# Kernel optimization log

Measured on AMD Instinct MI355X. Metric: run time of the kernel, lower is better.

## Reference

```python
import jax, jax.numpy as jnp
import numpy as np

B, N, C_IN, C_OUT = 32, 4096, 16, 64
EMB, LINK, WIN = 16, 3, 12


def setup_inputs() -> dict:
    key = jax.random.key(0)
    ks = jax.random.split(key, 7)
    s = lambda k, shape, sc=1.0: jax.random.normal(k, shape, dtype=jnp.float32) * sc
    return {
        "x": s(ks[0], (B, N, C_IN)),
        "x_window": s(ks[1], (B, WIN, N, C_IN)),
        "node_embeddings": s(ks[2], (N, EMB)),
        "weights_pool": s(ks[3], (EMB, LINK, C_IN, C_OUT), 0.1),
        "weights_window": s(ks[4], (EMB, C_IN, C_OUT), 0.1),
        "bias_pool": s(ks[5], (EMB, C_OUT), 0.1),
        "T": s(ks[6], (WIN,), 0.1),
    }


def reference(x, x_window, node_embeddings, weights_pool, weights_window, bias_pool, T):
    # Adaptive adjacency: softmax over rows of relu(E E^T)   [N, N]
    n = node_embeddings.shape[0]
    supports = jax.nn.softmax(
        jax.nn.relu(node_embeddings @ node_embeddings.T), axis=1)
    # Chebyshev polynomial hops: T0=I, T1=A, Tk = 2*A*T(k-1) - T(k-2)
    support_set = [jnp.eye(n, dtype=supports.dtype), supports]
    for _ in range(2, weights_pool.shape[1]):
        support_set.append(2.0 * (supports @ support_set[-1]) - support_set[-2])
    supports_k = jnp.stack(support_set, axis=0)  # [K, N, N]

    # Per-node weight generation from node embeddings
    weights = jnp.einsum('nd,dkio->nkio', node_embeddings, weights_pool)  # [N,K,Cin,Cout]
    bias = node_embeddings @ bias_pool  # [N, Cout]

    # Multi-hop spatial graph convolution
    x_g = jnp.einsum('knm,bmc->bnkc', supports_k, x)  # [B, N, K, Cin]
    x_gconv = jnp.einsum('bnki,nkio->bno', x_g, weights) + bias  # [B, N, Cout]

    # Temporal window transformation: time-mix with T, per-node weights
    x_w = jnp.einsum('btni,t->bni', x_window, T)  # [B, N, Cin]
    w_win = jnp.einsum('nd,dio->nio', node_embeddings, weights_window)  # [N,Cin,Cout]
    x_wconv = jnp.einsum('bni,nio->bno', x_w, w_win)  # [B, N, Cout]

    return x_gconv + x_wconv
```

## Files before the change

kernel.cpp:

```cpp
#include <hip/hip_runtime.h>
#include <hip/hip_bf16.h>

#define NN 4096
#define BB 32
#define CIN 16
#define COUT 64
#define EMB 16
#define KLINK 3
#define WWIN 12
#define BCIN (BB * CIN)
#define KSPLIT 4

typedef unsigned short ushort_t;
typedef __attribute__((ext_vector_type(8))) short bf16x8;
typedef __attribute__((ext_vector_type(4))) float f32x4;
typedef __attribute__((ext_vector_type(4))) unsigned short us4;
typedef __attribute__((ext_vector_type(8))) unsigned short us8;

static __device__ __forceinline__ ushort_t f2bf(float f) {
  union { float f; unsigned u; } v; v.f = f;
  const unsigned r = v.u + 0x7fffu + ((v.u >> 16) & 1u);
  return (ushort_t)(r >> 16);
}
static __device__ __forceinline__ float bf2f(ushort_t u) {
  union { unsigned u; float f; } v; v.u = ((unsigned)u) << 16;
  return v.f;
}

__device__ __forceinline__ void gload16(const void* g, void* l) {
  __builtin_amdgcn_global_load_lds(
      (const __attribute__((address_space(1))) void*)g,
      (__attribute__((address_space(3))) void*)l, 16, 0, 0);
}

__global__ __launch_bounds__(256) void prep_kernel(
    const float* __restrict__ E, const float* __restrict__ Wp,
    const float* __restrict__ Wwp, const float* __restrict__ biasp,
    ushort_t* __restrict__ Ebf, ushort_t* __restrict__ Wpct,
    float* __restrict__ biasn, float* __restrict__ r) {
  const int gid = blockIdx.x * 256 + threadIdx.x;
  if (gid < NN) {
    r[gid] = 0.0f;
    const float* e = E + (size_t)gid * EMB;
    ushort_t* o = Ebf + (size_t)gid * 32;
    #pragma unroll
    for (int d = 0; d < 16; ++d) o[d] = f2bf(e[d]);
    #pragma unroll
    for (int d = 16; d < 32; ++d) o[d] = 0;
  } else if (gid < 2 * NN) {
    const int j = gid - NN;
    const int oo = j >> 6;
    const int i = j & 63;
    const int q = i >> 4;
    const int ii = i & 15;
    ushort_t* w = Wpct + (size_t)j * 32;
    #pragma unroll
    for (int d = 0; d < 16; ++d) {
      float v;
      if (q == 0)
        v = Wp[((size_t)(d * 3 + 0) * 16 + ii) * 64 + oo] -
            Wp[((size_t)(d * 3 + 2) * 16 + ii) * 64 + oo];
      else if (q == 1)
        v = Wp[((size_t)(d * 3 + 1) * 16 + ii) * 64 + oo];
      else if (q == 2)
        v = 2.0f * Wp[((size_t)(d * 3 + 2) * 16 + ii) * 64 + oo];
      else
        v = Wwp[((size_t)d * 16 + ii) * 64 + oo];
      w[d] = f2bf(v);
    }
    #pragma unroll
    for (int d = 16; d < 32; ++d) w[d] = 0;
  } else {
    const int t = gid - 2 * NN;
    if (t < NN * 16) {
      const int n = t >> 4;
      const int o4 = t & 15;
      const float4* bp4 = reinterpret_cast<const float4*>(biasp);
      float4 acc = make_float4(0.f, 0.f, 0.f, 0.f);
      #pragma unroll
      for (int d = 0; d < 16; ++d) {
        const float e = E[(size_t)n * EMB + d];
        const float4 b = bp4[d * 16 + o4];
        acc.x += e * b.x; acc.y += e * b.y; acc.z += e * b.z; acc.w += e * b.w;
      }
      *reinterpret_cast<float4*>(biasn + (size_t)n * 64 + o4 * 4) = acc;
    }
  }
}

__global__ __launch_bounds__(256) void gemm_mfma_kernel(
    const ushort_t* __restrict__ Ag, const ushort_t* __restrict__ Bt,
    ushort_t* __restrict__ Ct, int lda, int ldb, int ldc, int Kdim,
    const float* __restrict__ rowR, const float* __restrict__ colR) {
  __shared__ ushort_t As[128 * 32];
  __shared__ ushort_t Bs[64 * 32];
  const int tid = threadIdx.x;
  const int lane = tid & 63;
  const int wid = tid >> 6;
  const int wr = wid >> 1;
  const int wc = wid & 1;
  const int row0 = blockIdx.y * 128;
  const int col0 = blockIdx.x * 64;

  f32x4 acc[4][2];
  #pragma unroll
  for (int i = 0; i < 4; ++i)
    #pragma unroll
    for (int j = 0; j < 2; ++j) acc[i][j] = (f32x4){0.f, 0.f, 0.f, 0.f};

  const int sr = tid >> 2;
  const int scs = (((tid & 3) ^ (sr & 3)) * 8);
  const ushort_t* agp0 = Ag + (size_t)(row0 + sr) * lda + scs;
  const ushort_t* agp1 = Ag + (size_t)(row0 + 64 + sr) * lda + scs;
  const ushort_t* bgp  = Bt + (size_t)(col0 + sr) * ldb + scs;
  ushort_t* asl0 = &As[tid * 8];
  ushort_t* asl1 = &As[2048 + tid * 8];
  ushort_t* bsl  = &Bs[tid * 8];

  const int kq = (lane >> 4) * 8;
  const int fr = lane & 15;

  for (int kb = 0; kb < Kdim; kb += 32) {
    gload16(agp0 + kb, asl0);
    gload16(agp1 + kb, asl1);
    gload16(bgp + kb, bsl);
    __syncthreads();

    bf16x8 af[4], bfr[2];
    #pragma unroll
    for (int i = 0; i < 4; ++i) {
      const int r = wr * 64 + i * 16 + fr;
      af[i] = *reinterpret_cast<const bf16x8*>(&As[r * 32 + (kq ^ ((r & 3) * 8))]);
    }
    #pragma unroll
    for (int j = 0; j < 2; ++j) {
      const int r = wc * 32 + j * 16 + fr;
      bfr[j] = *reinterpret_cast<const bf16x8*>(&Bs[r * 32 + (kq ^ ((r & 3) * 8))]);
    }
    #pragma unroll
    for (int i = 0; i < 4; ++i)
      #pragma unroll
      for (int j = 0; j < 2; ++j)
        acc[i][j] = __builtin_amdgcn_mfma_f32_16x16x32_bf16(af[i], bfr[j],
                                                            acc[i][j], 0, 0, 0);
    __syncthreads();
  }

  #pragma unroll
  for (int i = 0; i < 4; ++i) {
    const int rg = row0 + wr * 64 + i * 16 + ((lane >> 4) << 2);
    float4 ri = make_float4(1.f, 1.f, 1.f, 1.f);
    if (rowR) {
      const float4 rv = *reinterpret_cast<const float4*>(&rowR[rg]);
      ri.x = 1.0f / rv.x; ri.y = 1.0f / rv.y;
      ri.z = 1.0f / rv.z; ri.w = 1.0f / rv.w;
    }
    #pragma unroll
    for (int j = 0; j < 2; ++j) {
      const int cg = col0 + wc * 32 + j * 16 + (lane & 15);
      float cs = 1.0f;
      if (colR) cs = 1.0f / colR[cg];
      us4 o;
      o.x = f2bf(acc[i][j][0] * ri.x * cs);
      o.y = f2bf(acc[i][j][1] * ri.y * cs);
      o.z = f2bf(acc[i][j][2] * ri.z * cs);
      o.w = f2bf(acc[i][j][3] * ri.w * cs);
      *reinterpret_cast<us4*>(&Ct[(size_t)cg * ldc + rg]) = o;
    }
  }
}

__global__ __launch_bounds__(256) void gemm_splitk_kernel(
    const ushort_t* __restrict__ Ag, const ushort_t* __restrict__ Bt,
    float* __restrict__ Cp, int lda, int ldb, int ldc, int kchunk) {
  __shared__ ushort_t As[2][128 * 32];
  __shared__ ushort_t Bs[2][64 * 32];
  const int tid = threadIdx.x;
  const int lane = tid & 63;
  const int wid = tid >> 6;
  const int wr = wid >> 1;
  const int wc = wid & 1;

  const int gx = gridDim.x, gy = gridDim.y;
  const int nwg = gx * gy * gridDim.z;
  int L = blockIdx.x + gx * (blockIdx.y + gy * blockIdx.z);
  L = (L & 7) * (nwg >> 3) + (L >> 3);
  const int bx = L % gx;
  const int by = (L / gx) % gy;
  const int bz = L / (gx * gy);

  const int row0 = by * 128;
  const int col0 = bx * 64;
  const int kbase = bz * kchunk;

  f32x4 acc[4][2];
  #pragma unroll
  for (int i = 0; i < 4; ++i)
    #pragma unroll
    for (int j = 0; j < 2; ++j) acc[i][j] = (f32x4){0.f, 0.f, 0.f, 0.f};

  const int sr = tid >> 2;
  const int scs = (((tid & 3) ^ (sr & 3)) * 8);
  const ushort_t* agp0 = Ag + (size_t)(row0 + sr) * lda + scs;
  const ushort_t* agp1 = Ag + (size_t)(row0 + 64 + sr) * lda + scs;
  const ushort_t* bgp  = Bt + (size_t)(col0 + sr) * ldb + scs;

  const int kq = (lane >> 4) * 8;
  const int fr = lane & 15;
  const int nt = kchunk >> 5;

  gload16(agp0 + kbase, &As[0][tid * 8]);
  gload16(agp1 + kbase, &As[0][2048 + tid * 8]);
  gload16(bgp + kbase, &Bs[0][tid * 8]);
  __syncthreads();

  int cur = 0;
  #pragma unroll 2
  for (int t = 0; t < nt; ++t) {
    const int nxt = cur ^ 1;
    if (t + 1 < nt) {
      const int kb = kbase + (t + 1) * 32;
      gload16(agp0 + kb, &As[nxt][tid * 8]);
      gload16(agp1 + kb, &As[nxt][2048 + tid * 8]);
      gload16(bgp + kb, &Bs[nxt][tid * 8]);
    }
    bf16x8 af[4], bfr[2];
    #pragma unroll
    for (int i = 0; i < 4; ++i) {
      const int r = wr * 64 + i * 16 + fr;
      af[i] = *reinterpret_cast<const bf16x8*>(
          &As[cur][r * 32 + (kq ^ ((r & 3) * 8))]);
    }
    #pragma unroll
    for (int j = 0; j < 2; ++j) {
      const int r = wc * 32 + j * 16 + fr;
      bfr[j] = *reinterpret_cast<const bf16x8*>(
          &Bs[cur][r * 32 + (kq ^ ((r & 3) * 8))]);
    }
    #pragma unroll
    for (int i = 0; i < 4; ++i)
      #pragma unroll
      for (int j = 0; j < 2; ++j)
        acc[i][j] = __builtin_amdgcn_mfma_f32_16x16x32_bf16(af[i], bfr[j],
                                                            acc[i][j], 0, 0, 0);
    __syncthreads();
    cur = nxt;
  }

  float* cpz = Cp + (size_t)bz * ((size_t)BCIN * NN);
  #pragma unroll
  for (int i = 0; i < 4; ++i) {
    const int rg = row0 + wr * 64 + i * 16 + ((lane >> 4) << 2);
    #pragma unroll
    for (int j = 0; j < 2; ++j) {
      const int cg = col0 + wc * 32 + j * 16 + (lane & 15);
      *reinterpret_cast<f32x4*>(&cpz[(size_t)cg * ldc + rg]) = acc[i][j];
    }
  }
}

__global__ __launch_bounds__(256) void reduce_splitk_kernel(
    const float* __restrict__ Cp, ushort_t* __restrict__ Ct,
    const float* __restrict__ R, int mode) {
  const size_t e = ((size_t)blockIdx.x * 256 + threadIdx.x) << 2;
  const size_t SS = (size_t)BCIN * NN;
  float4 s = *reinterpret_cast<const float4*>(Cp + e);
  #pragma unroll
  for (int z = 1; z < KSPLIT; ++z) {
    const float4 v = *reinterpret_cast<const float4*>(Cp + (size_t)z * SS + e);
    s.x += v.x; s.y += v.y; s.z += v.z; s.w += v.w;
  }
  if (mode == 0) {
    const float4 rv = *reinterpret_cast<const float4*>(R + (e & (NN - 1)));
    s.x /= rv.x; s.y /= rv.y; s.z /= rv.z; s.w /= rv.w;
  } else {
    const float ri = 1.0f / R[e >> 9];
    s.x *= ri; s.y *= ri; s.z *= ri; s.w *= ri;
  }
  us4 o;
  o.x = f2bf(s.x); o.y = f2bf(s.y); o.z = f2bf(s.z); o.w = f2bf(s.w);
  *reinterpret_cast<us4*>(Ct + e) = o;
}

__global__ __launch_bounds__(256) void pgemm_kernel(
    const ushort_t* __restrict__ Ebf, ushort_t* __restrict__ Pb,
    float* __restrict__ r) {
  __shared__ ushort_t As[128 * 32];
  __shared__ ushort_t Bs[64 * 32];
  const int tid = threadIdx.x;
  const int lane = tid & 63;
  const int wid = tid >> 6;
  const int wr = wid >> 1;
  const int wc = wid & 1;
  const int row0 = blockIdx.y * 128;
  const int col0 = blockIdx.x * 64;

  const int sr = tid >> 2;
  const int scs = (((tid & 3) ^ (sr & 3)) * 8);
  gload16(Ebf + (size_t)(row0 + sr) * 32 + scs, &As[tid * 8]);
  gload16(Ebf + (size_t)(row0 + 64 + sr) * 32 + scs, &As[2048 + tid * 8]);
  gload16(Ebf + (size_t)(col0 + sr) * 32 + scs, &Bs[tid * 8]);
  __syncthreads();

  const int kq = (lane >> 4) * 8;
  const int fr = lane & 15;
  bf16x8 af[4], bfr[2];
  #pragma unroll
  for (int i = 0; i < 4; ++i) {
    const int rr = wr * 64 + i * 16 + fr;
    af[i] = *reinterpret_cast<const bf16x8*>(&As[rr * 32 + (kq ^ ((rr & 3) * 8))]);
  }
  #pragma unroll
  for (int j = 0; j < 2; ++j) {
    const int rr = wc * 32 + j * 16 + fr;
    bfr[j] = *reinterpret_cast<const bf16x8*>(&Bs[rr * 32 + (kq ^ ((rr & 3) * 8))]);
  }
  f32x4 acc[4][2];
  #pragma unroll
  for (int i = 0; i < 4; ++i)
    #pragma unroll
    for (int j = 0; j < 2; ++j) acc[i][j] = (f32x4){0.f, 0.f, 0.f, 0.f};
  #pragma unroll
  for (int i = 0; i < 4; ++i)
    #pragma unroll
    for (int j = 0; j < 2; ++j)
      acc[i][j] = __builtin_amdgcn_mfma_f32_16x16x32_bf16(af[i], bfr[j],
                                                          acc[i][j], 0, 0, 0);

  float pv[4][2][4];
  #pragma unroll
  for (int i = 0; i < 4; ++i) {
    const int rg = row0 + wr * 64 + i * 16 + ((lane >> 4) << 2);
    #pragma unroll
    for (int j = 0; j < 2; ++j) {
      const int cg = col0 + wc * 32 + j * 16 + (lane & 15);
      us4 o;
      #pragma unroll
      for (int q = 0; q < 4; ++q) {
        const float p = __expf(fmaxf(acc[i][j][q], 0.0f) - 16.0f);
        pv[i][j][q] = p;
        o[q] = f2bf(p);
      }
      *reinterpret_cast<us4*>(&Pb[(size_t)cg * NN + rg]) = o;
    }
  }
  #pragma unroll
  for (int i = 0; i < 4; ++i) {
    const int rg = row0 + wr * 64 + i * 16 + ((lane >> 4) << 2);
    #pragma unroll
    for (int q = 0; q < 4; ++q) {
      float s = pv[i][0][q] + pv[i][1][q];
      s += __shfl_xor(s, 1, 64);
      s += __shfl_xor(s, 2, 64);
      s += __shfl_xor(s, 4, 64);
      s += __shfl_xor(s, 8, 64);
      if ((lane & 15) == 0) atomicAdd(&r[rg + q], s);
    }
  }
}

__global__ __launch_bounds__(256) void transpose_x_kernel(
    const float* __restrict__ x, ushort_t* __restrict__ XtT) {
  __shared__ ushort_t T[16][72];
  const int b = blockIdx.y;
  const int m0 = blockIdx.x * 64;
  const int tid = threadIdx.x;
  const int i = tid & 15;
  const int ml = tid >> 4;
  #pragma unroll
  for (int it = 0; it < 4; ++it) {
    const int m = m0 + ml + it * 16;
    T[i][ml + it * 16] = f2bf(x[((size_t)b * NN + m) * CIN + i]);
  }
  __syncthreads();
  if (tid < 128) {
    const int r = tid >> 3;
    const int c8 = (tid & 7) * 8;
    const us8 v = *reinterpret_cast<const us8*>(&T[r][c8]);
    *reinterpret_cast<us8*>(&XtT[(size_t)(b * CIN + r) * NN + m0 + c8]) = v;
  }
}

__global__ __launch_bounds__(256) void transpose_y1_kernel(
    const ushort_t* __restrict__ Y1T, ushort_t* __restrict__ Y1n) {
  __shared__ ushort_t T[64][72];
  const int c0 = blockIdx.x * 64;
  const int r0 = blockIdx.y * 64;
  const int tid = threadIdx.x;
  #pragma unroll
  for (int t = 0; t < 2; ++t) {
    const int lin = tid + t * 256;
    const int row = lin >> 3;
    const int ch = lin & 7;
    const us8 v = *reinterpret_cast<const us8*>(
        Y1T + (size_t)(r0 + row) * NN + c0 + ch * 8);
    *reinterpret_cast<us8*>(&T[row][ch * 8]) = v;
  }
  __syncthreads();
  #pragma unroll
  for (int t = 0; t < 2; ++t) {
    const int lin = tid + t * 256;
    const int cc = lin >> 3;
    const int ch = lin & 7;
    us8 v;
    #pragma unroll
    for (int e = 0; e < 8; ++e) v[e] = T[ch * 8 + e][cc];
    *reinterpret_cast<us8*>(Y1n + (size_t)(c0 + cc) * BCIN + r0 + ch * 8) = v;
  }
}

__global__ __launch_bounds__(256) void time_mix_kernel(
    const float* __restrict__ xw, const float* __restrict__ Tv,
    float* __restrict__ XW) {
  const int idx = blockIdx.x * 256 + threadIdx.x;
  if (idx >= BB * NN * 4) return;
  const int c4 = (idx & 3) << 2;
  const int nn = (idx >> 2) & (NN - 1);
  const int b = idx >> 14;
  float4 acc = make_float4(0.f, 0.f, 0.f, 0.f);
  #pragma unroll
  for (int t = 0; t < WWIN; ++t) {
    const float4 v = *reinterpret_cast<const float4*>(
        xw + (((size_t)b * WWIN + t) * NN + nn) * CIN + c4);
    const float tv = Tv[t];
    acc.x += v.x * tv;
    acc.y += v.y * tv;
    acc.z += v.z * tv;
    acc.w += v.w * tv;
  }
  *reinterpret_cast<float4*>(XW + ((size_t)b * NN + nn) * CIN + c4) = acc;
}

__global__ __launch_bounds__(256) void combine_kernel(
    const float* __restrict__ x, const ushort_t* __restrict__ Y1n,
    const ushort_t* __restrict__ Y2n, const float* __restrict__ XW,
    const ushort_t* __restrict__ Wall, const float* __restrict__ biasn,
    float* __restrict__ out) {
  __shared__ ushort_t lds[4 * 6144];
  const int tid = threadIdx.x;
  const int lane = tid & 63;
  const int w = tid >> 6;
  ushort_t* Wl = lds + w * 6144;
  ushort_t* Vl = Wl + 4096;

  const int perm = ((lane >> 3) << 3) | ((lane & 7) ^ (lane >> 3));
  const int vb = lane >> 1;
  const int i0 = (lane & 1) * 8;

  for (int it = 0; it < 2; ++it) {
    const int n = blockIdx.x * 8 + w * 2 + it;
    asm volatile("s_waitcnt lgkmcnt(0)" ::: "memory");

    const ushort_t* wrow = Wall + (size_t)n * 4096;
    #pragma unroll
    for (int q = 0; q < 8; ++q)
      gload16(wrow + q * 512 + perm * 8, Wl + q * 512);

    const float4* xp = reinterpret_cast<const float4*>(
        x + ((size_t)vb * NN + n) * CIN + i0);
    const float4 xa = xp[0], xb = xp[1];
    const us8 y1 = *reinterpret_cast<const us8*>(Y1n + (size_t)n * BCIN + lane * 8);
    const us8 y2 = *reinterpret_cast<const us8*>(Y2n + (size_t)n * BCIN + lane * 8);
    const float4* xwp = reinterpret_cast<const float4*>(
        XW + ((size_t)vb * NN + n) * CIN + i0);
    const float4 wa = xwp[0], wb = xwp[1];
    us8 xv, wv;
    xv[0] = f2bf(xa.x); xv[1] = f2bf(xa.y); xv[2] = f2bf(xa.z); xv[3] = f2bf(xa.w);
    xv[4] = f2bf(xb.x); xv[5] = f2bf(xb.y); xv[6] = f2bf(xb.z); xv[7] = f2bf(xb.w);
    wv[0] = f2bf(wa.x); wv[1] = f2bf(wa.y); wv[2] = f2bf(wa.z); wv[3] = f2bf(wa.w);
    wv[4] = f2bf(wb.x); wv[5] = f2bf(wb.y); wv[6] = f2bf(wb.z); wv[7] = f2bf(wb.w);
    const int c0 = (lane & 1);
    const int vswz = vb & 7;
    *reinterpret_cast<us8*>(Vl + vb * 64 + (((c0 + 0) ^ vswz) << 3)) = xv;
    *reinterpret_cast<us8*>(Vl + vb * 64 + (((c0 + 2) ^ vswz) << 3)) = y1;
    *reinterpret_cast<us8*>(Vl + vb * 64 + (((c0 + 4) ^ vswz) << 3)) = y2;
    *reinterpret_cast<us8*>(Vl + vb * 64 + (((c0 + 6) ^ vswz) << 3)) = wv;

    f32x4 acc[2][4];
    #pragma unroll
    for (int nt = 0; nt < 4; ++nt) {
      const float bv = biasn[(size_t)n * 64 + nt * 16 + (lane & 15)];
      acc[0][nt] = (f32x4){bv, bv, bv, bv};
      acc[1][nt] = (f32x4){bv, bv, bv, bv};
    }

    asm volatile("s_waitcnt vmcnt(0)" ::: "memory");

    bf16x8 af[2][2], bfr[4][2];
    #pragma unroll
    for (int mt = 0; mt < 2; ++mt)
      #pragma unroll
      for (int kt = 0; kt < 2; ++kt) {
        const int rr = mt * 16 + (lane & 15);
        const int c = kt * 4 + (lane >> 4);
        af[mt][kt] = *reinterpret_cast<const bf16x8*>(
            Vl + rr * 64 + ((c ^ (lane & 7)) << 3));
      }
    #pragma unroll
    for (int nt = 0; nt < 4; ++nt)
      #pragma unroll
      for (int kt = 0; kt < 2; ++kt) {
        const int o = nt * 16 + (lane & 15);
        const int c = kt * 4 + (lane >> 4);
        bfr[nt][kt] = *reinterpret_cast<const bf16x8*>(
            Wl + o * 64 + ((c ^ (lane & 7)) << 3));
      }
    #pragma unroll
    for (int mt = 0; mt < 2; ++mt)
      #pragma unroll
      for (int nt = 0; nt < 4; ++nt)
        #pragma unroll
        for (int kt = 0; kt < 2; ++kt)
          acc[mt][nt] = __builtin_amdgcn_mfma_f32_16x16x32_bf16(
              af[mt][kt], bfr[nt][kt], acc[mt][nt], 0, 0, 0);

    #pragma unroll
    for (int mt = 0; mt < 2; ++mt)
      #pragma unroll
      for (int nt = 0; nt < 4; ++nt) {
        const int o = nt * 16 + (lane & 15);
        #pragma unroll
        for (int rr = 0; rr < 4; ++rr) {
          const int b = mt * 16 + ((lane >> 4) << 2) + rr;
          out[((size_t)b * NN + n) * COUT + o] = acc[mt][nt][rr];
        }
      }
  }
}

extern "C" void kernel_launch(void* const* d_in, const int* in_sizes, int n_in,
                              void* d_out, int out_size, void* d_ws,
                              size_t ws_size, hipStream_t stream) {
  const float* x = (const float*)d_in[0];
  const float* x_window = (const float*)d_in[1];
  const float* E = (const float*)d_in[2];
  const float* Wp = (const float*)d_in[3];
  const float* Wwp = (const float*)d_in[4];
  const float* biasp = (const float*)d_in[5];
  const float* Tv = (const float*)d_in[6];
  float* out = (float*)d_out;

  char* p = (char*)d_ws;
  float* XW = (float*)p;                 p += (size_t)BB * NN * CIN * 4;
  ushort_t* Pb = (ushort_t*)p;           p += (size_t)NN * NN * 2;
  ushort_t* XtT = (ushort_t*)p;          p += (size_t)BCIN * NN * 2;
  ushort_t* Y1T = (ushort_t*)p;          p += (size_t)BCIN * NN * 2;
  ushort_t* Y2n = (ushort_t*)p;          p += (size_t)NN * BCIN * 2;
  ushort_t* Y1n = (ushort_t*)p;          p += (size_t)NN * BCIN * 2;
  ushort_t* Wall = (ushort_t*)p;         p += (size_t)NN * 4096 * 2;
  ushort_t* Ebf = (ushort_t*)p;          p += (size_t)NN * 32 * 2;
  ushort_t* Wpct = (ushort_t*)p;         p += (size_t)NN * 32 * 2;
  float* biasn = (float*)p;              p += (size_t)NN * 64 * 4;
  float* r = (float*)p;                  p += (size_t)NN * 4;
  float* Cpart = (float*)p;              p += (size_t)KSPLIT * BCIN * NN * 4;

  prep_kernel<<<(2 * NN + NN * 16 + 255) / 256, 256, 0, stream>>>(
      E, Wp, Wwp, biasp, Ebf, Wpct, biasn, r);
  gemm_mfma_kernel<<<dim3(NN / 64, NN / 128), 256, 0, stream>>>(
      Wpct, Ebf, Wall, 32, 32, NN, 32, nullptr, nullptr);
  pgemm_kernel<<<dim3(NN / 64, NN / 128), 256, 0, stream>>>(Ebf, Pb, r);
  transpose_x_kernel<<<dim3(NN / 64, BB), 256, 0, stream>>>(x, XtT);
  gemm_splitk_kernel<<<dim3(BCIN / 64, NN / 128, KSPLIT), 256, 0, stream>>>(
      Pb, XtT, Cpart, NN, NN, NN, NN / KSPLIT);
  reduce_splitk_kernel<<<(BCIN * NN / 4) / 256, 256, 0, stream>>>(
      Cpart, Y1T, r, 0);
  gemm_splitk_kernel<<<dim3(NN / 64, BCIN / 128, KSPLIT), 256, 0, stream>>>(
      Y1T, Pb, Cpart, NN, NN, BCIN, NN / KSPLIT);
  reduce_splitk_kernel<<<(BCIN * NN / 4) / 256, 256, 0, stream>>>(
      Cpart, Y2n, r, 1);
  transpose_y1_kernel<<<dim3(NN / 64, BCIN / 64), 256, 0, stream>>>(Y1T, Y1n);
  time_mix_kernel<<<(BB * NN * 4 + 255) / 256, 256, 0, stream>>>(x_window, Tv, XW);
  combine_kernel<<<NN / 8, 256, 0, stream>>>(x, Y1n, Y2n, XW, Wall, biasn, out);
}
```

Measured before the change: 194.5 us.

## Triple-buffer split-K GEMM pipeline and fuse prep, transpose and reduce kernels

The split-K bf16 GEMM moves from a double-buffered loop to a three-stage LDS ring with explicit vmcnt waits and barriers, so loads for two tiles ahead overlap compute. The prep, x-transpose and time-mix kernels are merged into one front kernel, and the Y1 transpose is folded into the first split-K reduction. This cuts the launch count and one full read/write pass over Y1. It costs more LDS per block, which may reduce occupancy, and the hand-written wait counts must match the number of outstanding loads.

New measurement: 186.0 us. -4.4%, faster.

```diff
diff --git a/kernel.cpp b/kernel.cpp
--- a/kernel.cpp
+++ b/kernel.cpp
@@ -10,6 +10,8 @@
 #define WWIN 12
 #define BCIN (BB * CIN)
 #define KSPLIT 4
+#define KCHUNK (NN / KSPLIT)
+#define NT (KCHUNK / 32)
 
 typedef unsigned short ushort_t;
 typedef __attribute__((ext_vector_type(8))) short bf16x8;
@@ -22,10 +24,6 @@
   const unsigned r = v.u + 0x7fffu + ((v.u >> 16) & 1u);
   return (ushort_t)(r >> 16);
 }
-static __device__ __forceinline__ float bf2f(ushort_t u) {
-  union { unsigned u; float f; } v; v.u = ((unsigned)u) << 16;
-  return v.f;
-}
 
 __device__ __forceinline__ void gload16(const void* g, void* l) {
   __builtin_amdgcn_global_load_lds(
@@ -33,65 +31,107 @@
       (__attribute__((address_space(3))) void*)l, 16, 0, 0);
 }
 
-__global__ __launch_bounds__(256) void prep_kernel(
+__global__ __launch_bounds__(256) void front_kernel(
     const float* __restrict__ E, const float* __restrict__ Wp,
     const float* __restrict__ Wwp, const float* __restrict__ biasp,
+    const float* __restrict__ x, const float* __restrict__ xw,
+    const float* __restrict__ Tv,
     ushort_t* __restrict__ Ebf, ushort_t* __restrict__ Wpct,
-    float* __restrict__ biasn, float* __restrict__ r) {
-  const int gid = blockIdx.x * 256 + threadIdx.x;
-  if (gid < NN) {
-    r[gid] = 0.0f;
-    const float* e = E + (size_t)gid * EMB;
-    ushort_t* o = Ebf + (size_t)gid * 32;
-    #pragma unroll
-    for (int d = 0; d < 16; ++d) o[d] = f2bf(e[d]);
-    #pragma unroll
-    for (int d = 16; d < 32; ++d) o[d] = 0;
-  } else if (gid < 2 * NN) {
-    const int j = gid - NN;
-    const int oo = j >> 6;
-    const int i = j & 63;
-    const int q = i >> 4;
-    const int ii = i & 15;
-    ushort_t* w = Wpct + (size_t)j * 32;
-    #pragma unroll
-    for (int d = 0; d < 16; ++d) {
-      float v;
-      if (q == 0)
-        v = Wp[((size_t)(d * 3 + 0) * 16 + ii) * 64 + oo] -
-            Wp[((size_t)(d * 3 + 2) * 16 + ii) * 64 + oo];
-      else if (q == 1)
-        v = Wp[((size_t)(d * 3 + 1) * 16 + ii) * 64 + oo];
-      else if (q == 2)
-        v = 2.0f * Wp[((size_t)(d * 3 + 2) * 16 + ii) * 64 + oo];
-      else
-        v = Wwp[((size_t)d * 16 + ii) * 64 + oo];
-      w[d] = f2bf(v);
-    }
-    #pragma unroll
-    for (int d = 16; d < 32; ++d) w[d] = 0;
+    float* __restrict__ biasn, float* __restrict__ r,
+    ushort_t* __restrict__ XtT, float* __restrict__ XW) {
+  __shared__ ushort_t T[16][72];
+  const int bid = blockIdx.x;
+  const int tid = threadIdx.x;
+  if (bid < 288) {
+    const int gid = bid * 256 + tid;
+    if (gid < NN) {
+      r[gid] = 0.0f;
+      const float* e = E + (size_t)gid * EMB;
+      ushort_t* o = Ebf + (size_t)gid * 32;
+      #pragma unroll
+      for (int d = 0; d < 16; ++d) o[d] = f2bf(e[d]);
+      #pragma unroll
+      for (int d = 16; d < 32; ++d) o[d] = 0;
+    } else if (gid < 2 * NN) {
+      const int j = gid - NN;
+      const int oo = j >> 6;
+      const int i = j & 63;
+      const int q = i >> 4;
+      const int ii = i & 15;
+      ushort_t* w = Wpct + (size_t)j * 32;
+      #pragma unroll
+      for (int d = 0; d < 16; ++d) {
+        float v;
+        if (q == 0)
+          v = Wp[((size_t)(d * 3 + 0) * 16 + ii) * 64 + oo] -
+              Wp[((size_t)(d * 3 + 2) * 16 + ii) * 64 + oo];
+        else if (q == 1)
+          v = Wp[((size_t)(d * 3 + 1) * 16 + ii) * 64 + oo];
+        else if (q == 2)
+          v = 2.0f * Wp[((size_t)(d * 3 + 2) * 16 + ii) * 64 + oo];
+        else
+          v = Wwp[((size_t)d * 16 + ii) * 64 + oo];
+        w[d] = f2bf(v);
+      }
+      #pragma unroll
+      for (int d = 16; d < 32; ++d) w[d] = 0;
+    } else {
+      const int t = gid - 2 * NN;
+      if (t < NN * 16) {
+        const int n = t >> 4;
+        const int o4 = t & 15;
+        const float4* bp4 = reinterpret_cast<const float4*>(biasp);
+        float4 acc = make_float4(0.f, 0.f, 0.f, 0.f);
+        #pragma unroll
+        for (int d = 0; d < 16; ++d) {
+          const float e = E[(size_t)n * EMB + d];
+          const float4 b = bp4[d * 16 + o4];
+          acc.x += e * b.x; acc.y += e * b.y; acc.z += e * b.z; acc.w += e * b.w;
+        }
+        *reinterpret_cast<float4*>(biasn + (size_t)n * 64 + o4 * 4) = acc;
+      }
+    }
+  } else if (bid < 288 + 2048) {
+    const int bx = bid - 288;
+    const int b = bx >> 6;
+    const int m0 = (bx & 63) * 64;
+    const int i = tid & 15;
+    const int ml = tid >> 4;
+    #pragma unroll
+    for (int it = 0; it < 4; ++it) {
+      const int m = m0 + ml + it * 16;
+      T[i][ml + it * 16] = f2bf(x[((size_t)b * NN + m) * CIN + i]);
+    }
+    __syncthreads();
+    if (tid < 128) {
+      const int rr = tid >> 3;
+      const int c8 = (tid & 7) * 8;
+      const us8 v = *reinterpret_cast<const us8*>(&T[rr][c8]);
+      *reinterpret_cast<us8*>(&XtT[(size_t)(b * CIN + rr) * NN + m0 + c8]) = v;
+    }
   } else {
-    const int t = gid - 2 * NN;
-    if (t < NN * 16) {
-      const int n = t >> 4;
-      const int o4 = t & 15;
-      const float4* bp4 = reinterpret_cast<const float4*>(biasp);
-      float4 acc = make_float4(0.f, 0.f, 0.f, 0.f);
-      #pragma unroll
-      for (int d = 0; d < 16; ++d) {
-        const float e = E[(size_t)n * EMB + d];
-        const float4 b = bp4[d * 16 + o4];
-        acc.x += e * b.x; acc.y += e * b.y; acc.z += e * b.z; acc.w += e * b.w;
-      }
-      *reinterpret_cast<float4*>(biasn + (size_t)n * 64 + o4 * 4) = acc;
-    }
+    const int idx = (bid - 2336) * 256 + tid;
+    const int c4 = (idx & 3) << 2;
+    const int nn = (idx >> 2) & (NN - 1);
+    const int b = idx >> 14;
+    float4 acc = make_float4(0.f, 0.f, 0.f, 0.f);
+    #pragma unroll
+    for (int t = 0; t < WWIN; ++t) {
+      const float4 v = *reinterpret_cast<const float4*>(
+          xw + (((size_t)b * WWIN + t) * NN + nn) * CIN + c4);
+      const float tv = Tv[t];
+      acc.x += v.x * tv;
+      acc.y += v.y * tv;
+      acc.z += v.z * tv;
+      acc.w += v.w * tv;
+    }
+    *reinterpret_cast<float4*>(XW + ((size_t)b * NN + nn) * CIN + c4) = acc;
   }
 }
 
 __global__ __launch_bounds__(256) void gemm_mfma_kernel(
     const ushort_t* __restrict__ Ag, const ushort_t* __restrict__ Bt,
-    ushort_t* __restrict__ Ct, int lda, int ldb, int ldc, int Kdim,
-    const float* __restrict__ rowR, const float* __restrict__ colR) {
+    ushort_t* __restrict__ Ct, int lda, int ldb, int ldc, int Kdim) {
   __shared__ ushort_t As[128 * 32];
   __shared__ ushort_t Bs[64 * 32];
   const int tid = threadIdx.x;
@@ -149,32 +189,49 @@
   #pragma unroll
   for (int i = 0; i < 4; ++i) {
     const int rg = row0 + wr * 64 + i * 16 + ((lane >> 4) << 2);
-    float4 ri = make_float4(1.f, 1.f, 1.f, 1.f);
-    if (rowR) {
-      const float4 rv = *reinterpret_cast<const float4*>(&rowR[rg]);
-      ri.x = 1.0f / rv.x; ri.y = 1.0f / rv.y;
-      ri.z = 1.0f / rv.z; ri.w = 1.0f / rv.w;
-    }
     #pragma unroll
     for (int j = 0; j < 2; ++j) {
       const int cg = col0 + wc * 32 + j * 16 + (lane & 15);
-      float cs = 1.0f;
-      if (colR) cs = 1.0f / colR[cg];
       us4 o;
-      o.x = f2bf(acc[i][j][0] * ri.x * cs);
-      o.y = f2bf(acc[i][j][1] * ri.y * cs);
-      o.z = f2bf(acc[i][j][2] * ri.z * cs);
-      o.w = f2bf(acc[i][j][3] * ri.w * cs);
+      o.x = f2bf(acc[i][j][0]);
+      o.y = f2bf(acc[i][j][1]);
+      o.z = f2bf(acc[i][j][2]);
+      o.w = f2bf(acc[i][j][3]);
       *reinterpret_cast<us4*>(&Ct[(size_t)cg * ldc + rg]) = o;
     }
   }
+}
+
+template <int CUR>
+__device__ __forceinline__ void compute_tile(
+    const ushort_t (&As)[3][128 * 32], const ushort_t (&Bs)[3][64 * 32],
+    f32x4 (&acc)[4][2], int wr, int wc, int kq, int fr) {
+  bf16x8 af[4], bfr[2];
+  #pragma unroll
+  for (int i = 0; i < 4; ++i) {
+    const int rr = wr * 64 + i * 16 + fr;
+    af[i] = *reinterpret_cast<const bf16x8*>(
+        &As[CUR][rr * 32 + (kq ^ ((rr & 3) * 8))]);
+  }
+  #pragma unroll
+  for (int j = 0; j < 2; ++j) {
+    const int rr = wc * 32 + j * 16 + fr;
+    bfr[j] = *reinterpret_cast<const bf16x8*>(
+        &Bs[CUR][rr * 32 + (kq ^ ((rr & 3) * 8))]);
+  }
+  #pragma unroll
+  for (int i = 0; i < 4; ++i)
+    #pragma unroll
+    for (int j = 0; j < 2; ++j)
+      acc[i][j] = __builtin_amdgcn_mfma_f32_16x16x32_bf16(af[i], bfr[j],
+                                                          acc[i][j], 0, 0, 0);
 }
 
 __global__ __launch_bounds__(256) void gemm_splitk_kernel(
     const ushort_t* __restrict__ Ag, const ushort_t* __restrict__ Bt,
-    float* __restrict__ Cp, int lda, int ldb, int ldc, int kchunk) {
-  __shared__ ushort_t As[2][128 * 32];
-  __shared__ ushort_t Bs[2][64 * 32];
+    float* __restrict__ Cp, int lda, int ldb, int ldc) {
+  __shared__ ushort_t As[3][128 * 32];
+  __shared__ ushort_t Bs[3][64 * 32];
   const int tid = threadIdx.x;
   const int lane = tid & 63;
   const int wid = tid >> 6;
@@ -191,7 +248,7 @@
 
   const int row0 = by * 128;
   const int col0 = bx * 64;
-  const int kbase = bz * kchunk;
+  const int kbase = bz * KCHUNK;
 
   f32x4 acc[4][2];
   #pragma unroll
@@ -207,45 +264,43 @@
 
   const int kq = (lane >> 4) * 8;
   const int fr = lane & 15;
-  const int nt = kchunk >> 5;
-
-  gload16(agp0 + kbase, &As[0][tid * 8]);
-  gload16(agp1 + kbase, &As[0][2048 + tid * 8]);
-  gload16(bgp + kbase, &Bs[0][tid * 8]);
-  __syncthreads();
-
-  int cur = 0;
-  #pragma unroll 2
-  for (int t = 0; t < nt; ++t) {
-    const int nxt = cur ^ 1;
-    if (t + 1 < nt) {
-      const int kb = kbase + (t + 1) * 32;
-      gload16(agp0 + kb, &As[nxt][tid * 8]);
-      gload16(agp1 + kb, &As[nxt][2048 + tid * 8]);
-      gload16(bgp + kb, &Bs[nxt][tid * 8]);
-    }
-    bf16x8 af[4], bfr[2];
-    #pragma unroll
-    for (int i = 0; i < 4; ++i) {
-      const int r = wr * 64 + i * 16 + fr;
-      af[i] = *reinterpret_cast<const bf16x8*>(
-          &As[cur][r * 32 + (kq ^ ((r & 3) * 8))]);
-    }
-    #pragma unroll
-    for (int j = 0; j < 2; ++j) {
-      const int r = wc * 32 + j * 16 + fr;
-      bfr[j] = *reinterpret_cast<const bf16x8*>(
-          &Bs[cur][r * 32 + (kq ^ ((r & 3) * 8))]);
-    }
-    #pragma unroll
-    for (int i = 0; i < 4; ++i)
-      #pragma unroll
-      for (int j = 0; j < 2; ++j)
-        acc[i][j] = __builtin_amdgcn_mfma_f32_16x16x32_bf16(af[i], bfr[j],
-                                                            acc[i][j], 0, 0, 0);
-    __syncthreads();
-    cur = nxt;
-  }
+
+#define STAGE(BUF, KB)                              \
+  gload16(agp0 + (KB), &As[BUF][tid * 8]);          \
+  gload16(agp1 + (KB), &As[BUF][2048 + tid * 8]);   \
+  gload16(bgp + (KB), &Bs[BUF][tid * 8]);
+
+#define PIPE_STEP(CUR, NB, TT)                                  \
+  STAGE(NB, kbase + ((TT) + 2) * 32);                           \
+  asm volatile("s_waitcnt vmcnt(6)" ::: "memory");              \
+  __builtin_amdgcn_s_barrier();                                 \
+  __builtin_amdgcn_sched_barrier(0);                            \
+  compute_tile<CUR>(As, Bs, acc, wr, wc, kq, fr);               \
+  __builtin_amdgcn_sched_barrier(0);                            \
+  __builtin_amdgcn_s_barrier();
+
+  STAGE(0, kbase);
+  STAGE(1, kbase + 32);
+
+  for (int tt = 0; tt < (NT - 2) / 3; ++tt) {
+    const int t3 = tt * 3;
+    PIPE_STEP(0, 2, t3 + 0);
+    PIPE_STEP(1, 0, t3 + 1);
+    PIPE_STEP(2, 1, t3 + 2);
+  }
+  asm volatile("s_waitcnt vmcnt(3)" ::: "memory");
+  __builtin_amdgcn_s_barrier();
+  __builtin_amdgcn_sched_barrier(0);
+  compute_tile<0>(As, Bs, acc, wr, wc, kq, fr);
+  __builtin_amdgcn_sched_barrier(0);
+  __builtin_amdgcn_s_barrier();
+  asm volatile("s_waitcnt vmcnt(0)" ::: "memory");
+  __builtin_amdgcn_s_barrier();
+  __builtin_amdgcn_sched_barrier(0);
+  compute_tile<1>(As, Bs, acc, wr, wc, kq, fr);
+
+#undef PIPE_STEP
+#undef STAGE
 
   float* cpz = Cp + (size_t)bz * ((size_t)BCIN * NN);
   #pragma unroll
@@ -259,9 +314,49 @@
   }
 }
 
-__global__ __launch_bounds__(256) void reduce_splitk_kernel(
+__global__ __launch_bounds__(256) void reduce_y1_kernel(
+    const float* __restrict__ Cp, const float* __restrict__ R,
+    ushort_t* __restrict__ Y1T, ushort_t* __restrict__ Y1n) {
+  __shared__ ushort_t T[64][72];
+  const int n0 = blockIdx.x * 64;
+  const int bc0 = blockIdx.y * 64;
+  const int tid = threadIdx.x;
+  const size_t SS = (size_t)BCIN * NN;
+  #pragma unroll
+  for (int q = 0; q < 4; ++q) {
+    const int lin = tid + q * 256;
+    const int bc = lin >> 4;
+    const int nc = (lin & 15) * 4;
+    const size_t base = (size_t)(bc0 + bc) * NN + n0 + nc;
+    float4 s = *reinterpret_cast<const float4*>(Cp + base);
+    #pragma unroll
+    for (int z = 1; z < KSPLIT; ++z) {
+      const float4 v = *reinterpret_cast<const float4*>(Cp + (size_t)z * SS + base);
+      s.x += v.x; s.y += v.y; s.z += v.z; s.w += v.w;
+    }
+    const float4 rv = *reinterpret_cast<const float4*>(R + n0 + nc);
+    us4 o;
+    o.x = f2bf(s.x / rv.x); o.y = f2bf(s.y / rv.y);
+    o.z = f2bf(s.z / rv.z); o.w = f2bf(s.w / rv.w);
+    *reinterpret_cast<us4*>(&Y1T[base]) = o;
+    *reinterpret_cast<us4*>(&T[bc][nc]) = o;
+  }
+  __syncthreads();
+  #pragma unroll
+  for (int t = 0; t < 2; ++t) {
+    const int lin = tid + t * 256;
+    const int nr = lin >> 3;
+    const int ch = lin & 7;
+    us8 v;
+    #pragma unroll
+    for (int e = 0; e < 8; ++e) v[e] = T[ch * 8 + e][nr];
+    *reinterpret_cast<us8*>(&Y1n[(size_t)(n0 + nr) * BCIN + bc0 + ch * 8]) = v;
+  }
+}
+
+__global__ __launch_bounds__(256) void reduce_y2_kernel(
     const float* __restrict__ Cp, ushort_t* __restrict__ Ct,
-    const float* __restrict__ R, int mode) {
+    const float* __restrict__ R) {
   const size_t e = ((size_t)blockIdx.x * 256 + threadIdx.x) << 2;
   const size_t SS = (size_t)BCIN * NN;
   float4 s = *reinterpret_cast<const float4*>(Cp + e);
@@ -270,13 +365,8 @@
     const float4 v = *reinterpret_cast<const float4*>(Cp + (size_t)z * SS + e);
     s.x += v.x; s.y += v.y; s.z += v.z; s.w += v.w;
   }
-  if (mode == 0) {
-    const float4 rv = *reinterpret_cast<const float4*>(R + (e & (NN - 1)));
-    s.x /= rv.x; s.y /= rv.y; s.z /= rv.z; s.w /= rv.w;
-  } else {
-    const float ri = 1.0f / R[e >> 9];
-    s.x *= ri; s.y *= ri; s.z *= ri; s.w *= ri;
-  }
+  const float ri = 1.0f / R[e >> 9];
+  s.x *= ri; s.y *= ri; s.z *= ri; s.w *= ri;
   us4 o;
   o.x = f2bf(s.x); o.y = f2bf(s.y); o.z = f2bf(s.z); o.w = f2bf(s.w);
   *reinterpret_cast<us4*>(Ct + e) = o;
@@ -357,78 +447,6 @@
       if ((lane & 15) == 0) atomicAdd(&r[rg + q], s);
     }
   }
-}
-
-__global__ __launch_bounds__(256) void transpose_x_kernel(
-    const float* __restrict__ x, ushort_t* __restrict__ XtT) {
-  __shared__ ushort_t T[16][72];
-  const int b = blockIdx.y;
-  const int m0 = blockIdx.x * 64;
-  const int tid = threadIdx.x;
-  const int i = tid & 15;
-  const int ml = tid >> 4;
-  #pragma unroll
-  for (int it = 0; it < 4; ++it) {
-    const int m = m0 + ml + it * 16;
-    T[i][ml + it * 16] = f2bf(x[((size_t)b * NN + m) * CIN + i]);
-  }
-  __syncthreads();
-  if (tid < 128) {
-    const int r = tid >> 3;
-    const int c8 = (tid & 7) * 8;
-    const us8 v = *reinterpret_cast<const us8*>(&T[r][c8]);
-    *reinterpret_cast<us8*>(&XtT[(size_t)(b * CIN + r) * NN + m0 + c8]) = v;
-  }
-}
-
-__global__ __launch_bounds__(256) void transpose_y1_kernel(
-    const ushort_t* __restrict__ Y1T, ushort_t* __restrict__ Y1n) {
-  __shared__ ushort_t T[64][72];
-  const int c0 = blockIdx.x * 64;
-  const int r0 = blockIdx.y * 64;
-  const int tid = threadIdx.x;
-  #pragma unroll
-  for (int t = 0; t < 2; ++t) {
-    const int lin = tid + t * 256;
-    const int row = lin >> 3;
-    const int ch = lin & 7;
-    const us8 v = *reinterpret_cast<const us8*>(
-        Y1T + (size_t)(r0 + row) * NN + c0 + ch * 8);
-    *reinterpret_cast<us8*>(&T[row][ch * 8]) = v;
-  }
-  __syncthreads();
-  #pragma unroll
-  for (int t = 0; t < 2; ++t) {
-    const int lin = tid + t * 256;
-    const int cc = lin >> 3;
-    const int ch = lin & 7;
-    us8 v;
-    #pragma unroll
-    for (int e = 0; e < 8; ++e) v[e] = T[ch * 8 + e][cc];
-    *reinterpret_cast<us8*>(Y1n + (size_t)(c0 + cc) * BCIN + r0 + ch * 8) = v;
-  }
-}
-
-__global__ __launch_bounds__(256) void time_mix_kernel(
-    const float* __restrict__ xw, const float* __restrict__ Tv,
-    float* __restrict__ XW) {
-  const int idx = blockIdx.x * 256 + threadIdx.x;
-  if (idx >= BB * NN * 4) return;
-  const int c4 = (idx & 3) << 2;
-  const int nn = (idx >> 2) & (NN - 1);
-  const int b = idx >> 14;
-  float4 acc = make_float4(0.f, 0.f, 0.f, 0.f);
-  #pragma unroll
-  for (int t = 0; t < WWIN; ++t) {
-    const float4 v = *reinterpret_cast<const float4*>(
-        xw + (((size_t)b * WWIN + t) * NN + nn) * CIN + c4);
-    const float tv = Tv[t];
-    acc.x += v.x * tv;
-    acc.y += v.y * tv;
-    acc.z += v.z * tv;
-    acc.w += v.w * tv;
-  }
-  *reinterpret_cast<float4*>(XW + ((size_t)b * NN + nn) * CIN + c4) = acc;
 }
 
 __global__ __launch_bounds__(256) void combine_kernel(
@@ -554,21 +572,17 @@
   float* r = (float*)p;                  p += (size_t)NN * 4;
   float* Cpart = (float*)p;              p += (size_t)KSPLIT * BCIN * NN * 4;
 
-  prep_kernel<<<(2 * NN + NN * 16 + 255) / 256, 256, 0, stream>>>(
-      E, Wp, Wwp, biasp, Ebf, Wpct, biasn, r);
+  front_kernel<<<4384, 256, 0, stream>>>(E, Wp, Wwp, biasp, x, x_window, Tv,
+                                         Ebf, Wpct, biasn, r, XtT, XW);
   gemm_mfma_kernel<<<dim3(NN / 64, NN / 128), 256, 0, stream>>>(
-      Wpct, Ebf, Wall, 32, 32, NN, 32, nullptr, nullptr);
+      Wpct, Ebf, Wall, 32, 32, NN, 32);
   pgemm_kernel<<<dim3(NN / 64, NN / 128), 256, 0, stream>>>(Ebf, Pb, r);
-  transpose_x_kernel<<<dim3(NN / 64, BB), 256, 0, stream>>>(x, XtT);
   gemm_splitk_kernel<<<dim3(BCIN / 64, NN / 128, KSPLIT), 256, 0, stream>>>(
-      Pb, XtT, Cpart, NN, NN, NN, NN / KSPLIT);
-  reduce_splitk_kernel<<<(BCIN * NN / 4) / 256, 256, 0, stream>>>(
-      Cpart, Y1T, r, 0);
+      Pb, XtT, Cpart, NN, NN, NN);
+  reduce_y1_kernel<<<dim3(NN / 64, BCIN / 64), 256, 0, stream>>>(
+      Cpart, r, Y1T, Y1n);
   gemm_splitk_kernel<<<dim3(NN / 64, BCIN / 128, KSPLIT), 256, 0, stream>>>(
-      Y1T, Pb, Cpart, NN, NN, BCIN, NN / KSPLIT);
-  reduce_splitk_kernel<<<(BCIN * NN / 4) / 256, 256, 0, stream>>>(
-      Cpart, Y2n, r, 1);
-  transpose_y1_kernel<<<dim3(NN / 64, BCIN / 64), 256, 0, stream>>>(Y1T, Y1n);
-  time_mix_kernel<<<(BB * NN * 4 + 255) / 256, 256, 0, stream>>>(x_window, Tv, XW);
+      Y1T, Pb, Cpart, NN, NN, BCIN);
+  reduce_y2_kernel<<<(BCIN * NN / 4) / 256, 256, 0, stream>>>(Cpart, Y2n, r);
   combine_kernel<<<NN / 8, 256, 0, stream>>>(x, Y1n, Y2n, XW, Wall, biasn, out);
 }
```
